# Optimization experiments

Measured on AMD Instinct MI355X. Metric: run time of the kernel, lower is better.

Reference implementation:

```python
import jax, jax.numpy as jnp
import numpy as np

N_NODES = 100000
NEG_SLOPE = 0.2


def _gat_layer(x, src, dst, W, a_src, a_dst, b):
    """Single-head PyG-style GATConv (heads=1, concat, self-loops already in src/dst)."""
    h = x @ W                                   # [N, out]
    alpha_s = h @ a_src                          # [N]
    alpha_d = h @ a_dst                          # [N]
    e = jax.nn.leaky_relu(alpha_s[src] + alpha_d[dst], NEG_SLOPE)  # [E]
    # numerically stable softmax over incoming edges of each dst node
    m = jax.ops.segment_max(e, dst, num_segments=N_NODES)           # [N]
    ex = jnp.exp(e - m[dst])                                        # [E]
    denom = jax.ops.segment_sum(ex, dst, num_segments=N_NODES)      # [N]
    attn = ex / denom[dst]                                          # [E]
    out = jax.ops.segment_sum(h[src] * attn[:, None], dst, num_segments=N_NODES)
    return out + b


def setup_inputs() -> dict:
    key = jax.random.key(0)
    ks = jax.random.split(key, 16)
    F_IN, H1, H2 = 256, 64, 32
    E = 1600000
    x = jax.random.normal(ks[0], (N_NODES, F_IN), dtype=jnp.float32)
    edge_index = jax.random.randint(ks[1], (2, E), 0, N_NODES, dtype=jnp.int32)
    def glorot(k, shape):
        lim = float(np.sqrt(6.0 / (shape[0] + shape[-1])))
        return jax.random.uniform(k, shape, jnp.float32, -lim, lim)
    return {
        "x": x,
        "edge_index": edge_index,
        "W1": glorot(ks[2], (F_IN, H1)),
        "a_src1": glorot(ks[3], (H1,)),
        "a_dst1": glorot(ks[4], (H1,)),
        "b1": jnp.zeros((H1,), jnp.float32),
        "W2": glorot(ks[5], (H1, H2)),
        "a_src2": glorot(ks[6], (H2,)),
        "a_dst2": glorot(ks[7], (H2,)),
        "b2": jnp.zeros((H2,), jnp.float32),
        "Wfc": glorot(ks[8], (H2, 1)),
        "bfc": jnp.zeros((1,), jnp.float32),
    }


def reference(x, edge_index, W1, a_src1, a_dst1, b1, W2, a_src2, a_dst2, b2, Wfc, bfc):
    # add self loops (PyG GATConv default add_self_loops=True)
    loop = jnp.arange(N_NODES, dtype=edge_index.dtype)
    src = jnp.concatenate([edge_index[0], loop])
    dst = jnp.concatenate([edge_index[1], loop])
    h = jax.nn.relu(_gat_layer(x, src, dst, W1, a_src1, a_dst1, b1))
    h = jax.nn.relu(_gat_layer(h, src, dst, W2, a_src2, a_dst2, b2))
    return h @ Wfc + bfc  # [N, 1]
```

## Files before the change

### kernel.cpp

```cpp
#include <hip/hip_runtime.h>
#include <hip/hip_bf16.h>

#define NEG_SLOPE 0.2f
#define NINF (-1e30f)

#define BKT_BITS 7
#define BKT 128
#define PB 256

typedef __attribute__((ext_vector_type(8))) short s8v;
typedef __attribute__((ext_vector_type(4))) float f4v;

__device__ __forceinline__ unsigned short f2bf(float f) {
    unsigned u = __float_as_uint(f);
    u = (u + 0x7fffu + ((u >> 16) & 1u)) >> 16;
    return (unsigned short)u;
}
__device__ __forceinline__ float bf2f(unsigned short h) {
    return __uint_as_float(((unsigned)h) << 16);
}


__global__ __launch_bounds__(256) void hist_pb_k(
    const int* __restrict__ edst, int E, int Etot, int NBK, int EPB,
    int* __restrict__ counts)
{
    __shared__ int lh[1024];
    for (int i = threadIdx.x; i < NBK; i += 256) lh[i] = 0;
    __syncthreads();
    const int e0 = blockIdx.x * EPB;
    const int e1 = min(e0 + EPB, Etot);
    for (int i = e0 + threadIdx.x; i < e1; i += 256) {
        int d = (i < E) ? edst[i] : (i - E);
        atomicAdd(&lh[d >> BKT_BITS], 1);
    }
    __syncthreads();
    for (int b = threadIdx.x; b < NBK; b += 256)
        counts[b * PB + blockIdx.x] = lh[b];
}

__global__ __launch_bounds__(256) void scan_partial_k(
    const int* __restrict__ a, int L, int* __restrict__ partials)
{
    __shared__ int red[256];
    const int t = threadIdx.x;
    const int base = blockIdx.x * 1024 + t * 4;
    int sum = 0;
    #pragma unroll
    for (int k = 0; k < 4; ++k) {
        int i = base + k;
        if (i < L) sum += a[i];
    }
    red[t] = sum;
    __syncthreads();
    #pragma unroll
    for (int o = 128; o; o >>= 1) {
        if (t < o) red[t] += red[t + o];
        __syncthreads();
    }
    if (t == 0) partials[blockIdx.x] = red[0];
}

__global__ __launch_bounds__(256) void scan_partials_k(
    int* __restrict__ partials, int nb)
{
    __shared__ int sh[256];
    const int t = threadIdx.x;
    int v = (t < nb) ? partials[t] : 0;
    sh[t] = v;
    __syncthreads();
    #pragma unroll
    for (int o = 1; o < 256; o <<= 1) {
        int u = (t >= o) ? sh[t - o] : 0;
        __syncthreads();
        sh[t] += u;
        __syncthreads();
    }
    if (t < nb) partials[t] = sh[t] - v;
}

__global__ __launch_bounds__(256) void scan_final_k(
    int* __restrict__ a, const int* __restrict__ partials, int L)
{
    __shared__ int sh[256];
    const int t = threadIdx.x;
    const int base = blockIdx.x * 1024 + t * 4;
    int v[4];
    int sum = 0;
    #pragma unroll
    for (int k = 0; k < 4; ++k) {
        int i = base + k;
        v[k] = (i < L) ? a[i] : 0;
        sum += v[k];
    }
    sh[t] = sum;
    __syncthreads();
    #pragma unroll
    for (int o = 1; o < 256; o <<= 1) {
        int u = (t >= o) ? sh[t - o] : 0;
        __syncthreads();
        sh[t] += u;
        __syncthreads();
    }
    int run = sh[t] - sum + partials[blockIdx.x];
    #pragma unroll
    for (int k = 0; k < 4; ++k) {
        int i = base + k;
        if (i < L) a[i] = run;
        run += v[k];
    }
}

__global__ __launch_bounds__(256) void scatter_pb_k(
    const int* __restrict__ esrc, const int* __restrict__ edst,
    int E, int Etot, int NBK, int EPB,
    const int* __restrict__ cbase, unsigned* __restrict__ tmp)
{
    __shared__ int cur[1024];
    for (int b = threadIdx.x; b < NBK; b += 256)
        cur[b] = cbase[b * PB + blockIdx.x];
    __syncthreads();
    const int e0 = blockIdx.x * EPB;
    const int e1 = min(e0 + EPB, Etot);
    for (int i = e0 + threadIdx.x; i < e1; i += 256) {
        int d = (i < E) ? edst[i] : (i - E);
        int s = (i < E) ? esrc[i] : (i - E);
        int pos = atomicAdd(&cur[d >> BKT_BITS], 1);
        tmp[pos] = ((unsigned)s << BKT_BITS) | (unsigned)(d & (BKT - 1));
    }
}

__global__ __launch_bounds__(256) void bucket_finalize_k(
    const unsigned* __restrict__ tmp, const int* __restrict__ cbase,
    int N, int NBK, int Etot,
    int* __restrict__ rowptr, int* __restrict__ csr)
{
    __shared__ int cnt[BKT];
    __shared__ int off[BKT];
    const int b = blockIdx.x;
    const int t = threadIdx.x;
    const int start = cbase[b * PB];
    const int end = (b + 1 < NBK) ? cbase[(b + 1) * PB] : Etot;
    const int n0 = b << BKT_BITS;
    const int nn = min(BKT, N - n0);

    if (t < BKT) cnt[t] = 0;
    __syncthreads();
    for (int i = start + t; i < end; i += 256)
        atomicAdd(&cnt[tmp[i] & (BKT - 1)], 1);
    __syncthreads();
    if (t < BKT) off[t] = cnt[t];
    __syncthreads();
    #pragma unroll
    for (int o = 1; o < BKT; o <<= 1) {
        int u = (t >= o && t < BKT) ? off[t - o] : 0;
        __syncthreads();
        if (t < BKT) off[t] += u;
        __syncthreads();
    }
    if (t < BKT) {
        int ex = off[t] - cnt[t];
        if (t < nn) rowptr[n0 + t] = start + ex;
        cnt[t] = ex;
    }
    if (b == 0 && t == 0) rowptr[N] = Etot;
    __syncthreads();
    for (int i = start + t; i < end; i += 256) {
        unsigned w = tmp[i];
        int dl = w & (BKT - 1);
        int pos = atomicAdd(&cnt[dl], 1);
        csr[start + pos] = (int)(w >> BKT_BITS);
    }
}

__global__ __launch_bounds__(256) void prep_w_k(
    const float* __restrict__ W1, const float* __restrict__ W2,
    short* __restrict__ Wt1h, short* __restrict__ Wt1l,
    short* __restrict__ Wt2h, short* __restrict__ Wt2l)
{
    int t = blockIdx.x * 256 + threadIdx.x;
    if (t < 256 * 64) {
        int k = t >> 6, c = t & 63;
        float v = W1[t];
        unsigned short h = f2bf(v);
        unsigned short l = f2bf(v - bf2f(h));
        Wt1h[c * 256 + k] = (short)h;
        Wt1l[c * 256 + k] = (short)l;
    } else if (t < 256 * 64 + 64 * 32) {
        int e = t - 256 * 64;
        int k = e >> 5, c = e & 31;
        float v = W2[e];
        unsigned short h = f2bf(v);
        unsigned short l = f2bf(v - bf2f(h));
        Wt2h[c * 64 + k] = (short)h;
        Wt2l[c * 64 + k] = (short)l;
    }
}

template <int K, int M, bool RELU_BIAS>
__global__ __launch_bounds__(256) void gemm_mfma_k(
    const float* __restrict__ X,
    const short* __restrict__ Wth, const short* __restrict__ Wtl,
    const float* __restrict__ a_s, const float* __restrict__ a_d,
    const float* __restrict__ bias_in,
    unsigned short* __restrict__ Hb, float* __restrict__ AS, float* __restrict__ AD,
    int N)
{
    constexpr int NT = M / 16;
    constexpr int KS = K / 32;
    __shared__ short Xhi[2][64][40];
    __shared__ short Xlo[2][64][40];

    const int wave = threadIdx.x >> 6;
    const int lane = threadIdx.x & 63;
    const int lc = lane & 15;
    const int k8 = (lane >> 4) * 8;
    const int rb = blockIdx.x * 64;

    const int trow = threadIdx.x >> 2;
    const int tseg = (threadIdx.x & 3) * 8;
    const int gr = rb + trow;
    const bool rok = gr < N;
    const float* xrow = X + (long)gr * K + tseg;

    f4v acc[NT];
    #pragma unroll
    for (int c = 0; c < NT; ++c) acc[c] = (f4v){0.f, 0.f, 0.f, 0.f};

    float v[8];
    {
        if (rok) {
            float4 v0 = *(const float4*)(xrow);
            float4 v1 = *(const float4*)(xrow + 4);
            v[0] = v0.x; v[1] = v0.y; v[2] = v0.z; v[3] = v0.w;
            v[4] = v1.x; v[5] = v1.y; v[6] = v1.z; v[7] = v1.w;
        } else {
            #pragma unroll
            for (int j = 0; j < 8; ++j) v[j] = 0.f;
        }
        if (RELU_BIAS) {
            #pragma unroll
            for (int j = 0; j < 8; ++j) {
                float w = v[j] + bias_in[tseg + j];
                v[j] = w > 0.f ? w : 0.f;
            }
        }
        s8v hv, lv;
        #pragma unroll
        for (int j = 0; j < 8; ++j) {
            unsigned short h = f2bf(v[j]);
            hv[j] = (short)h;
            lv[j] = (short)f2bf(v[j] - bf2f(h));
        }
        *(s8v*)&Xhi[0][trow][tseg] = hv;
        *(s8v*)&Xlo[0][trow][tseg] = lv;
    }

    for (int ks = 0; ks < KS; ++ks) {
        float vn[8];
        if (ks + 1 < KS) {
            if (rok) {
                float4 v0 = *(const float4*)(xrow + (ks + 1) * 32);
                float4 v1 = *(const float4*)(xrow + (ks + 1) * 32 + 4);
                vn[0] = v0.x; vn[1] = v0.y; vn[2] = v0.z; vn[3] = v0.w;
                vn[4] = v1.x; vn[5] = v1.y; vn[6] = v1.z; vn[7] = v1.w;
            } else {
                #pragma unroll
                for (int j = 0; j < 8; ++j) vn[j] = 0.f;
            }
        }
        __syncthreads();

        const int arow = wave * 16 + lc;
        s8v ah = *(const s8v*)&Xhi[ks & 1][arow][k8];
        s8v al = *(const s8v*)&Xlo[ks & 1][arow][k8];
        #pragma unroll
        for (int c = 0; c < NT; ++c) {
            const long wo = (long)(c * 16 + lc) * K + ks * 32 + k8;
            s8v bh = *(const s8v*)(Wth + wo);
            s8v bl = *(const s8v*)(Wtl + wo);
            acc[c] = __builtin_amdgcn_mfma_f32_16x16x32_bf16(ah, bh, acc[c], 0, 0, 0);
            acc[c] = __builtin_amdgcn_mfma_f32_16x16x32_bf16(al, bh, acc[c], 0, 0, 0);
            acc[c] = __builtin_amdgcn_mfma_f32_16x16x32_bf16(ah, bl, acc[c], 0, 0, 0);
        }

        if (ks + 1 < KS) {
            if (RELU_BIAS) {
                #pragma unroll
                for (int j = 0; j < 8; ++j) {
                    float w = vn[j] + bias_in[(ks + 1) * 32 + tseg + j];
                    vn[j] = w > 0.f ? w : 0.f;
                }
            }
            s8v hv, lv;
            #pragma unroll
            for (int j = 0; j < 8; ++j) {
                unsigned short h = f2bf(vn[j]);
                hv[j] = (short)h;
                lv[j] = (short)f2bf(vn[j] - bf2f(h));
            }
            *(s8v*)&Xhi[(ks + 1) & 1][trow][tseg] = hv;
            *(s8v*)&Xlo[(ks + 1) & 1][trow][tseg] = lv;
        }
    }

    float ps[4] = {0.f, 0.f, 0.f, 0.f}, pd[4] = {0.f, 0.f, 0.f, 0.f};
    #pragma unroll
    for (int c = 0; c < NT; ++c) {
        float asv = a_s[c * 16 + lc];
        float adv = a_d[c * 16 + lc];
        #pragma unroll
        for (int j = 0; j < 4; ++j) {
            float hval = acc[c][j];
            int grow = rb + wave * 16 + (lane >> 4) * 4 + j;
            if (grow < N) Hb[(long)grow * M + c * 16 + lc] = f2bf(hval);
            ps[j] = fmaf(hval, asv, ps[j]);
            pd[j] = fmaf(hval, adv, pd[j]);
        }
    }
    #pragma unroll
    for (int j = 0; j < 4; ++j) {
        #pragma unroll
        for (int o = 8; o >= 1; o >>= 1) {
            ps[j] += __shfl_xor(ps[j], o);
            pd[j] += __shfl_xor(pd[j], o);
        }
    }
    if (lc == 0) {
        #pragma unroll
        for (int j = 0; j < 4; ++j) {
            int grow = rb + wave * 16 + (lane >> 4) * 4 + j;
            if (grow < N) { AS[grow] = ps[j]; AD[grow] = pd[j]; }
        }
    }
}

__global__ __launch_bounds__(256) void agg_csr_k(
    const int* __restrict__ rowptr, const int* __restrict__ csr_src,
    const float* __restrict__ as_, const float* __restrict__ ad_,
    const unsigned short* __restrict__ H, float* __restrict__ OUT, int N)
{
    constexpr int M = 64, LP = 32, EH = 2;
    __shared__ float lw[4][64];
    __shared__ int   ls[4][64];
    const int wave = threadIdx.x >> 6;
    const int lane = threadIdx.x & 63;
    const int d = blockIdx.x * 4 + wave;
    if (d >= N) return;
    const int r0 = rowptr[d];
    const int deg = rowptr[d + 1] - r0;
    const float adv = ad_[d];

    const int f2 = (lane % LP) * 2;
    const int eh = lane / LP;

    float m = NINF, den = 0.0f, acc0 = 0.0f, acc1 = 0.0f;
    for (int base = 0; base < deg; base += 64) {
        int j = base + lane;
        int s = 0;
        float e = NINF;
        if (j < deg) {
            s = csr_src[r0 + j];
            e = as_[s] + adv;
            e = e > 0.0f ? e : NEG_SLOPE * e;
        }
        float cm = e;
        #pragma unroll
        for (int o = 32; o; o >>= 1) cm = fmaxf(cm, __shfl_xor(cm, o));
        if (cm > m) {
            float sc = __expf(m - cm);
            acc0 *= sc; acc1 *= sc; den *= sc; m = cm;
        }
        float w = __expf(e - m);
        float wsum = w;
        #pragma unroll
        for (int o = 32; o; o >>= 1) wsum += __shfl_xor(wsum, o);
        den += wsum;
        lw[wave][lane] = w;
        ls[wave][lane] = s;
        int cnt = min(64, deg - base);
        #pragma unroll 4
        for (int jj = 0; jj < cnt; jj += EH) {
            int je = jj + eh;
            float wj = (je < cnt) ? lw[wave][je] : 0.0f;
            int   sj = (je < cnt) ? ls[wave][je] : 0;
            unsigned hv = *(const unsigned*)&H[(long)sj * M + f2];
            acc0 = fmaf(wj, bf2f((unsigned short)(hv & 0xffffu)), acc0);
            acc1 = fmaf(wj, bf2f((unsigned short)(hv >> 16)), acc1);
        }
    }
    #pragma unroll
    for (int o = LP; o < 64; o <<= 1) {
        acc0 += __shfl_xor(acc0, o);
        acc1 += __shfl_xor(acc1, o);
    }
    if (lane < LP) {
        float inv = 1.0f / den;
        *(float2*)&OUT[(long)d * M + f2] = make_float2(acc0 * inv, acc1 * inv);
    }
}

__global__ __launch_bounds__(256) void agg_fc_k(
    const int* __restrict__ rowptr, const int* __restrict__ csr_src,
    const float* __restrict__ as_, const float* __restrict__ ad_,
    const unsigned short* __restrict__ H,
    const float* __restrict__ b2, const float* __restrict__ Wfc,
    const float* __restrict__ bfc,
    float* __restrict__ out, int N)
{
    constexpr int M = 32, LP = 16, EH = 4;
    __shared__ float lw[4][64];
    __shared__ int   ls[4][64];
    const int wave = threadIdx.x >> 6;
    const int lane = threadIdx.x & 63;
    const int d = blockIdx.x * 4 + wave;
    if (d >= N) return;
    const int r0 = rowptr[d];
    const int deg = rowptr[d + 1] - r0;
    const float adv = ad_[d];

    const int f2 = (lane % LP) * 2;
    const int eh = lane / LP;

    float m = NINF, den = 0.0f, acc0 = 0.0f, acc1 = 0.0f;
    for (int base = 0; base < deg; base += 64) {
        int j = base + lane;
        int s = 0;
        float e = NINF;
        if (j < deg) {
            s = csr_src[r0 + j];
            e = as_[s] + adv;
            e = e > 0.0f ? e : NEG_SLOPE * e;
        }
        float cm = e;
        #pragma unroll
        for (int o = 32; o; o >>= 1) cm = fmaxf(cm, __shfl_xor(cm, o));
        if (cm > m) {
            float sc = __expf(m - cm);
            acc0 *= sc; acc1 *= sc; den *= sc; m = cm;
        }
        float w = __expf(e - m);
        float wsum = w;
        #pragma unroll
        for (int o = 32; o; o >>= 1) wsum += __shfl_xor(wsum, o);
        den += wsum;
        lw[wave][lane] = w;
        ls[wave][lane] = s;
        int cnt = min(64, deg - base);
        #pragma unroll 4
        for (int jj = 0; jj < cnt; jj += EH) {
            int je = jj + eh;
            float wj = (je < cnt) ? lw[wave][je] : 0.0f;
            int   sj = (je < cnt) ? ls[wave][je] : 0;
            unsigned hv = *(const unsigned*)&H[(long)sj * M + f2];
            acc0 = fmaf(wj, bf2f((unsigned short)(hv & 0xffffu)), acc0);
            acc1 = fmaf(wj, bf2f((unsigned short)(hv >> 16)), acc1);
        }
    }
    #pragma unroll
    for (int o = LP; o < 64; o <<= 1) {
        acc0 += __shfl_xor(acc0, o);
        acc1 += __shfl_xor(acc1, o);
    }
    float inv = 1.0f / den;
    float h0 = acc0 * inv + b2[f2];
    float h1 = acc1 * inv + b2[f2 + 1];
    h0 = h0 > 0.f ? h0 : 0.f;
    h1 = h1 > 0.f ? h1 : 0.f;
    float p = h0 * Wfc[f2] + h1 * Wfc[f2 + 1];
    #pragma unroll
    for (int o = 8; o >= 1; o >>= 1) p += __shfl_xor(p, o);
    if (lane == 0) out[d] = p + bfc[0];
}

extern "C" void kernel_launch(void* const* d_in, const int* in_sizes, int n_in,
                              void* d_out, int out_size, void* d_ws, size_t ws_size,
                              hipStream_t stream) {
    const float* x      = (const float*)d_in[0];
    const int*   eidx   = (const int*)d_in[1];
    const float* W1     = (const float*)d_in[2];
    const float* a_src1 = (const float*)d_in[3];
    const float* a_dst1 = (const float*)d_in[4];
    const float* b1     = (const float*)d_in[5];
    const float* W2     = (const float*)d_in[6];
    const float* a_src2 = (const float*)d_in[7];
    const float* a_dst2 = (const float*)d_in[8];
    const float* b2     = (const float*)d_in[9];
    const float* Wfc    = (const float*)d_in[10];
    const float* bfc    = (const float*)d_in[11];
    float* out = (float*)d_out;

    const int N = in_sizes[0] / 256;
    const int E = in_sizes[1] / 2;
    const int Etot = E + N;
    const int* esrc = eidx;
    const int* edst = eidx + E;
    const int NBK = (N + BKT - 1) >> BKT_BITS;
    const int EPB = (Etot + PB - 1) / PB;
    const int L   = NBK * PB;

    char* cur = (char*)d_ws;
    auto alloc = [&](size_t bytes) -> void* {
        void* r = (void*)cur;
        cur += (bytes + 255) & ~(size_t)255;
        return r;
    };
    int* rowptr   = (int*)alloc((size_t)(N + 1) * 4);
    int* counts   = (int*)alloc((size_t)L * 4);
    int* partials = (int*)alloc(1024);
    unsigned* tmp = (unsigned*)alloc((size_t)Etot * 4);
    int* csr      = (int*)alloc((size_t)Etot * 4);
    float* as1    = (float*)alloc((size_t)N * 4);
    float* ad1    = (float*)alloc((size_t)N * 4);
    float* as2    = (float*)alloc((size_t)N * 4);
    float* ad2    = (float*)alloc((size_t)N * 4);
    short* Wt1h   = (short*)alloc(16384 * 2);
    short* Wt1l   = (short*)alloc(16384 * 2);
    short* Wt2h   = (short*)alloc(2048 * 2);
    short* Wt2l   = (short*)alloc(2048 * 2);
    unsigned short* h1b = (unsigned short*)alloc((size_t)N * 64 * 2);
    unsigned short* h2b = (unsigned short*)alloc((size_t)N * 32 * 2);
    float* h1out  = (float*)alloc((size_t)N * 64 * 4);

    prep_w_k<<<72, 256, 0, stream>>>(W1, W2, Wt1h, Wt1l, Wt2h, Wt2l);
    {
        int nb1 = (L + 1023) / 1024;
        hist_pb_k<<<PB, 256, 0, stream>>>(edst, E, Etot, NBK, EPB, counts);
        scan_partial_k<<<nb1, 256, 0, stream>>>(counts, L, partials);
        scan_partials_k<<<1, 256, 0, stream>>>(partials, nb1);
        scan_final_k<<<nb1, 256, 0, stream>>>(counts, partials, L);
        scatter_pb_k<<<PB, 256, 0, stream>>>(esrc, edst, E, Etot, NBK, EPB, counts, tmp);
        bucket_finalize_k<<<NBK, 256, 0, stream>>>(tmp, counts, N, NBK, Etot, rowptr, csr);
    }

    const int gemmBlocks = (N + 63) / 64;
    const int aggBlocks  = (N + 3) / 4;

    gemm_mfma_k<256, 64, false><<<gemmBlocks, 256, 0, stream>>>(
        x, Wt1h, Wt1l, a_src1, a_dst1, nullptr, h1b, as1, ad1, N);
    agg_csr_k<<<aggBlocks, 256, 0, stream>>>(
        rowptr, csr, as1, ad1, h1b, h1out, N);

    gemm_mfma_k<64, 32, true><<<gemmBlocks, 256, 0, stream>>>(
        h1out, Wt2h, Wt2l, a_src2, a_dst2, b1, h2b, as2, ad2, N);

    agg_fc_k<<<aggBlocks, 256, 0, stream>>>(
        rowptr, csr, as2, ad2, h2b, b2, Wfc, bfc, out, N);
}
```

Baseline: 391.8 us.

## Stage GEMM input rows to LDS via direct global-to-LDS loads with swizzle

The MFMA GEMM kernel stops double-buffering pre-split bf16 hi/lo tiles through registers and block-wide barriers. Each wave now issues global_load_lds transfers that copy its whole 16-row fp32 slice straight into a per-wave LDS buffer, using an XOR-swizzled column layout to avoid bank conflicts. It then reads from LDS and does the bias/ReLU and bf16 hi/lo split per k-step in registers. This drops __syncthreads and register staging, but raises LDS use to 64 KB per block for K=256, which may limit occupancy. It also serialises the full load ahead of all compute instead of overlapping them.

```diff
diff --git a/kernel.cpp b/kernel.cpp
--- a/kernel.cpp
+++ b/kernel.cpp
@@ -208,72 +208,59 @@
 {
     constexpr int NT = M / 16;
     constexpr int KS = K / 32;
-    __shared__ short Xhi[2][64][40];
-    __shared__ short Xlo[2][64][40];
+    constexpr int CPR = K / 4;
+    constexpr int RPC = 64 / CPR;
+    constexpr int CALLS = 16 / RPC;
+    __shared__ float Xs[4][16][K];
 
     const int wave = threadIdx.x >> 6;
     const int lane = threadIdx.x & 63;
     const int lc = lane & 15;
-    const int k8 = (lane >> 4) * 8;
+    const int hi = lane >> 4;
+    const int k8 = hi * 8;
     const int rb = blockIdx.x * 64;
-
-    const int trow = threadIdx.x >> 2;
-    const int tseg = (threadIdx.x & 3) * 8;
-    const int gr = rb + trow;
-    const bool rok = gr < N;
-    const float* xrow = X + (long)gr * K + tseg;
+    const int rw = rb + wave * 16;
+
+    #pragma unroll
+    for (int i = 0; i < CALLS; ++i) {
+        int ri = i * RPC + lane / CPR;
+        int pc = lane % CPR;
+        int cg = (pc & ~7) | ((pc ^ ri) & 7);
+        int srow = min(rw + ri, N - 1);
+        const float* src = X + (long)srow * K + cg * 4;
+        void* ldst = (void*)&Xs[wave][i * RPC][0];
+        __builtin_amdgcn_global_load_lds(
+            (const __attribute__((address_space(1))) unsigned*)src,
+            (__attribute__((address_space(3))) unsigned*)ldst, 16, 0, 0);
+    }
+    asm volatile("s_waitcnt vmcnt(0)" ::: "memory");
+    __builtin_amdgcn_sched_barrier(0);
 
     f4v acc[NT];
     #pragma unroll
     for (int c = 0; c < NT; ++c) acc[c] = (f4v){0.f, 0.f, 0.f, 0.f};
 
-    float v[8];
-    {
-        if (rok) {
-            float4 v0 = *(const float4*)(xrow);
-            float4 v1 = *(const float4*)(xrow + 4);
-            v[0] = v0.x; v[1] = v0.y; v[2] = v0.z; v[3] = v0.w;
-            v[4] = v1.x; v[5] = v1.y; v[6] = v1.z; v[7] = v1.w;
-        } else {
-            #pragma unroll
-            for (int j = 0; j < 8; ++j) v[j] = 0.f;
-        }
+    #pragma unroll
+    for (int ks = 0; ks < KS; ++ks) {
+        const int j0 = ks * 8 + hi * 2;
+        const int p0 = (j0 & ~7) | ((j0 ^ lc) & 7);
+        float4 f0 = *(const float4*)&Xs[wave][lc][p0 * 4];
+        float4 f1 = *(const float4*)&Xs[wave][lc][(p0 ^ 1) * 4];
+        float v[8] = {f0.x, f0.y, f0.z, f0.w, f1.x, f1.y, f1.z, f1.w};
         if (RELU_BIAS) {
             #pragma unroll
             for (int j = 0; j < 8; ++j) {
-                float w = v[j] + bias_in[tseg + j];
+                float w = v[j] + bias_in[ks * 32 + k8 + j];
                 v[j] = w > 0.f ? w : 0.f;
             }
         }
-        s8v hv, lv;
+        s8v ah, al;
         #pragma unroll
         for (int j = 0; j < 8; ++j) {
             unsigned short h = f2bf(v[j]);
-            hv[j] = (short)h;
-            lv[j] = (short)f2bf(v[j] - bf2f(h));
-        }
-        *(s8v*)&Xhi[0][trow][tseg] = hv;
-        *(s8v*)&Xlo[0][trow][tseg] = lv;
-    }
-
-    for (int ks = 0; ks < KS; ++ks) {
-        float vn[8];
-        if (ks + 1 < KS) {
-            if (rok) {
-                float4 v0 = *(const float4*)(xrow + (ks + 1) * 32);
-                float4 v1 = *(const float4*)(xrow + (ks + 1) * 32 + 4);
-                vn[0] = v0.x; vn[1] = v0.y; vn[2] = v0.z; vn[3] = v0.w;
-                vn[4] = v1.x; vn[5] = v1.y; vn[6] = v1.z; vn[7] = v1.w;
-            } else {
-                #pragma unroll
-                for (int j = 0; j < 8; ++j) vn[j] = 0.f;
-            }
-        }
-        __syncthreads();
-
-        const int arow = wave * 16 + lc;
-        s8v ah = *(const s8v*)&Xhi[ks & 1][arow][k8];
-        s8v al = *(const s8v*)&Xlo[ks & 1][arow][k8];
+            ah[j] = (short)h;
+            al[j] = (short)f2bf(v[j] - bf2f(h));
+        }
         #pragma unroll
         for (int c = 0; c < NT; ++c) {
             const long wo = (long)(c * 16 + lc) * K + ks * 32 + k8;
@@ -283,25 +270,6 @@
             acc[c] = __builtin_amdgcn_mfma_f32_16x16x32_bf16(al, bh, acc[c], 0, 0, 0);
             acc[c] = __builtin_amdgcn_mfma_f32_16x16x32_bf16(ah, bl, acc[c], 0, 0, 0);
         }
-
-        if (ks + 1 < KS) {
-            if (RELU_BIAS) {
-                #pragma unroll
-                for (int j = 0; j < 8; ++j) {
-                    float w = vn[j] + bias_in[(ks + 1) * 32 + tseg + j];
-                    vn[j] = w > 0.f ? w : 0.f;
-                }
-            }
-            s8v hv, lv;
-            #pragma unroll
-            for (int j = 0; j < 8; ++j) {
-                unsigned short h = f2bf(vn[j]);
-                hv[j] = (short)h;
-                lv[j] = (short)f2bf(vn[j] - bf2f(h));
-            }
-            *(s8v*)&Xhi[(ks + 1) & 1][trow][tseg] = hv;
-            *(s8v*)&Xlo[(ks + 1) & 1][trow][tseg] = lv;
-        }
     }
 
     float ps[4] = {0.f, 0.f, 0.f, 0.f}, pd[4] = {0.f, 0.f, 0.f, 0.f};
@@ -312,7 +280,7 @@
         #pragma unroll
         for (int j = 0; j < 4; ++j) {
             float hval = acc[c][j];
-            int grow = rb + wave * 16 + (lane >> 4) * 4 + j;
+            int grow = rw + hi * 4 + j;
             if (grow < N) Hb[(long)grow * M + c * 16 + lc] = f2bf(hval);
             ps[j] = fmaf(hval, asv, ps[j]);
             pd[j] = fmaf(hval, adv, pd[j]);
@@ -329,7 +297,7 @@
     if (lc == 0) {
         #pragma unroll
         for (int j = 0; j < 4; ++j) {
-            int grow = rb + wave * 16 + (lane >> 4) * 4 + j;
+            int grow = rw + hi * 4 + j;
             if (grow < N) { AS[grow] = ps[j]; AD[grow] = pd[j]; }
         }
     }
```

Result: slower. 407.8 us (+4.1%).
